# Kernel optimization log

Measured on AMD Instinct MI355X. Metric: run time of the kernel, lower is better.

## Reference

```python
import jax, jax.numpy as jnp
import numpy as np

HEAD_DIM = 32

def setup_inputs() -> dict:
    key = jax.random.key(0)
    ks = jax.random.split(key, 6)
    B, H, W, C = 16, 64, 64, 512
    ws = 8
    n_heads = C // HEAD_DIM
    return {
        "x": jax.random.normal(ks[0], (B, H, W, C), dtype=jnp.float32),
        "w_qkv": jax.random.normal(ks[1], (C, 3 * C), dtype=jnp.float32) * 0.02,
        "b_qkv": jnp.zeros((3 * C,), dtype=jnp.float32),
        "rel_pos": jax.random.normal(ks[2], ((2 * ws - 1) ** 2, n_heads), dtype=jnp.float32) * 0.02,
        "w_out": jax.random.normal(ks[3], (C, C), dtype=jnp.float32) * 0.02,
        "b_out": jnp.zeros((C,), dtype=jnp.float32),
        "window_size": ws,
    }

def _rel_pos_index(p):
    # static numpy computation, identical to torch buffer construction
    coords = np.stack(np.meshgrid(np.arange(p), np.arange(p), indexing='ij')).reshape(2, -1)
    rel = (coords[:, :, None] - coords[:, None, :]).transpose(1, 2, 0)
    rel[:, :, 0] += p - 1
    rel[:, :, 1] += p - 1
    rel[:, :, 0] *= 2 * p - 1
    return rel.sum(-1)  # (p*p, p*p)

def reference(x, w_qkv, b_qkv, rel_pos, w_out, b_out, window_size):
    B, H, W, C = x.shape
    p = int(window_size)
    n = p * p
    n_heads = rel_pos.shape[1]
    hd = C // n_heads
    shift = p // 2
    # type == 'W': cyclic shift before windowing
    xs = jnp.roll(x, shift=(-shift, -shift), axis=(1, 2))
    nh, nw = H // p, W // p
    # window partition -> (B*nh*nw, n, C)
    xw = xs.reshape(B, nh, p, nw, p, C).transpose(0, 1, 3, 2, 4, 5).reshape(B * nh * nw, n, C)
    qkv = xw @ w_qkv + b_qkv                      # (Bw, n, 3C)
    qkv = qkv.reshape(-1, n, 3, n_heads, hd).transpose(2, 0, 3, 1, 4)  # (3, Bw, h, n, hd)
    q, k, v = qkv[0], qkv[1], qkv[2]
    idx = _rel_pos_index(p)
    bias = rel_pos[idx.reshape(-1)].reshape(n, n, n_heads).transpose(2, 0, 1)  # (h, n, n)
    scale = hd ** -0.5
    attn = jnp.einsum('bhqd,bhkd->bhqk', q * scale, k) + bias[None]
    attn = jax.nn.softmax(attn, axis=-1)
    out = jnp.einsum('bhqk,bhkd->bhqd', attn, v)  # (Bw, h, n, hd)
    out = out.transpose(0, 2, 1, 3).reshape(-1, n, C)
    out = out @ w_out + b_out                     # (Bw, n, C_out)
    Co = out.shape[-1]
    out = out.reshape(B, nh, nw, p, p, Co).transpose(0, 1, 3, 2, 4, 5).reshape(B, H, W, Co)
    return jnp.roll(out, shift=(shift, shift), axis=(1, 2))
```

## Files before the change

kernel.cpp:

```cpp
#include <hip/hip_runtime.h>
#include <hip/hip_bf16.h>
#include <stdint.h>

typedef __hip_bfloat16 bf16;
typedef __attribute__((ext_vector_type(8))) short short8;
typedef __attribute__((ext_vector_type(4))) float f32x4;

#define NWIN 1024
#define NH 16
#define HD 32
#define SHIFT 4

#define GLOAD_LDS16(gptr, lptr)                                                      \
    __builtin_amdgcn_global_load_lds(                                                \
        (const __attribute__((address_space(1))) void*)(gptr),                       \
        (__attribute__((address_space(3))) void*)(lptr), 16, 0, 0)

__device__ __forceinline__ int row_to_pixel(int r) {
    int win = r >> 6, t = r & 63;
    int b = win >> 6, wy = (win >> 3) & 7, wx = win & 7;
    int h = ((wy << 3) + (t >> 3) + SHIFT) & 63;
    int w = ((wx << 3) + (t & 7) + SHIFT) & 63;
    return (((b << 6) | h) << 6) | w;
}

__device__ __forceinline__ short f2bf_bits(float f) {
    bf16 h = __float2bfloat16(f);
    return *reinterpret_cast<short*>(&h);
}

__global__ void transpose_f2b(const float* __restrict__ src, short* __restrict__ dst,
                              int K, int N) {
    int idx = blockIdx.x * 256 + threadIdx.x;
    if (idx >= K * N) return;
    int k = idx / N, n = idx - k * N;
    dst[n * K + k] = f2bf_bits(src[idx]);
}

__global__ __launch_bounds__(256)
void gather_cast(const float* __restrict__ x, short* __restrict__ a) {
    int chunk = blockIdx.x * 256 + threadIdx.x;
    int r = chunk >> 6, c8 = (chunk & 63) << 3;
    int pix = row_to_pixel(r);
    const float* src = x + pix * 512 + c8;
    float4 f0 = *(const float4*)src;
    float4 f1 = *(const float4*)(src + 4);
    short8 v;
    v[0] = f2bf_bits(f0.x); v[1] = f2bf_bits(f0.y);
    v[2] = f2bf_bits(f0.z); v[3] = f2bf_bits(f0.w);
    v[4] = f2bf_bits(f1.x); v[5] = f2bf_bits(f1.y);
    v[6] = f2bf_bits(f1.z); v[7] = f2bf_bits(f1.w);
    *(short8*)(a + r * 512 + c8) = v;
}

__global__ __launch_bounds__(256, 4)
void qkv_gemm(const bf16* __restrict__ a, const bf16* __restrict__ wT,
              const float* __restrict__ bqkv, bf16* __restrict__ qkv) {
    __shared__ __align__(16) short As[128 * 32];
    __shared__ __align__(16) short Bs[128 * 32];
    const int tid = threadIdx.x;
    const int lane = tid & 63, wave = tid >> 6;
    const int wr = wave >> 1, wc = wave & 1;
    const int h = blockIdx.x;
    const int v = (h & 7) * 768 + (h >> 3);
    const int by = v / 12, bx = v - by * 12;
    const int m0 = by * 128, n0 = bx * 128;

    const int lrow = lane >> 2, lc8 = (lane & 3) << 3;
    const short* agA0 = (const short*)a + (m0 + wave * 16 + lrow) * 512 + lc8;
    const short* agA1 = (const short*)a + (m0 + (wave + 4) * 16 + lrow) * 512 + lc8;
    const short* bgB0 = (const short*)wT + (n0 + wave * 16 + lrow) * 512 + lc8;
    const short* bgB1 = (const short*)wT + (n0 + (wave + 4) * 16 + lrow) * 512 + lc8;
    short* ldsA0 = As + wave * 512;
    short* ldsA1 = As + (wave + 4) * 512;
    short* ldsB0 = Bs + wave * 512;
    short* ldsB1 = Bs + (wave + 4) * 512;

    f32x4 acc[4][4] = {};
    for (int k0 = 0; k0 < 512; k0 += 32) {
        __syncthreads();
        GLOAD_LDS16(agA0 + k0, ldsA0);
        GLOAD_LDS16(agA1 + k0, ldsA1);
        GLOAD_LDS16(bgB0 + k0, ldsB0);
        GLOAD_LDS16(bgB1 + k0, ldsB1);
        __syncthreads();
        const int kk = (lane >> 4) << 3;
        short8 af[4], bfr[4];
#pragma unroll
        for (int mt = 0; mt < 4; ++mt)
            af[mt] = *(const short8*)&As[(wr * 64 + mt * 16 + (lane & 15)) * 32 + kk];
#pragma unroll
        for (int nt = 0; nt < 4; ++nt)
            bfr[nt] = *(const short8*)&Bs[(wc * 64 + nt * 16 + (lane & 15)) * 32 + kk];
#pragma unroll
        for (int mt = 0; mt < 4; ++mt)
#pragma unroll
            for (int nt = 0; nt < 4; ++nt)
                acc[mt][nt] = __builtin_amdgcn_mfma_f32_16x16x32_bf16(af[mt], bfr[nt],
                                                                      acc[mt][nt], 0, 0, 0);
    }

#pragma unroll
    for (int mt = 0; mt < 4; ++mt) {
        int r0 = m0 + wr * 64 + mt * 16 + ((lane >> 4) << 2);
        int win = r0 >> 6, t0 = r0 & 63;
#pragma unroll
        for (int nt = 0; nt < 4; ++nt) {
            int c = n0 + wc * 64 + nt * 16 + (lane & 15);
            int which = c >> 9, head = (c >> 5) & 15, d = c & 31;
            float bias = bqkv[c];
            float scale = (which == 0) ? 0.17677669529663689f : 1.0f;
            short* p = (short*)qkv + (((which * NWIN + win) * NH + head) * 64 + t0) * HD + d;
#pragma unroll
            for (int reg = 0; reg < 4; ++reg)
                p[reg * HD] = f2bf_bits((acc[mt][nt][reg] + bias) * scale);
        }
    }
}

__global__ __launch_bounds__(256, 4)
void attn_kernel(bf16* __restrict__ qkv, const float* __restrict__ relpos) {
    const int win = blockIdx.x, head = blockIdx.y;
    __shared__ __align__(16) short qs[64 * 40];
    __shared__ __align__(16) short ks[64 * 40];
    __shared__ __align__(16) short vT[32 * 72];
    __shared__ __align__(16) short Ps[64 * 72];
    __shared__ float rel[225];
    const int tid = threadIdx.x, lane = tid & 63, wave = tid >> 6;
    const int base = (win * NH + head) * 2048;
    const short* qg = (const short*)qkv + base;
    const short* kg = qg + NWIN * NH * 2048;
    const short* vg = kg + NWIN * NH * 2048;

    {
        int row = tid >> 2, c8 = (tid & 3) << 3;
        *(short8*)&qs[row * 40 + c8] = *(const short8*)(qg + row * 32 + c8);
        *(short8*)&ks[row * 40 + c8] = *(const short8*)(kg + row * 32 + c8);
        short8 vv = *(const short8*)(vg + row * 32 + c8);
#pragma unroll
        for (int e = 0; e < 8; ++e) vT[(c8 + e) * 72 + row] = vv[e];
    }
    if (tid < 225) rel[tid] = relpos[tid * 16 + head];
    __syncthreads();

    {
        const int kk = (lane >> 4) << 3;
        short8 aq = *(const short8*)&qs[(wave * 16 + (lane & 15)) * 40 + kk];
        f32x4 sacc[4];
#pragma unroll
        for (int nt = 0; nt < 4; ++nt) {
            short8 bk = *(const short8*)&ks[(nt * 16 + (lane & 15)) * 40 + kk];
            f32x4 z = {};
            sacc[nt] = __builtin_amdgcn_mfma_f32_16x16x32_bf16(aq, bk, z, 0, 0, 0);
        }
#pragma unroll
        for (int reg = 0; reg < 4; ++reg) {
            int qt = wave * 16 + ((lane >> 4) << 2) + reg;
            float pv[4];
            float m = -3e38f;
#pragma unroll
            for (int nt = 0; nt < 4; ++nt) {
                int kt = nt * 16 + (lane & 15);
                int idx = ((qt >> 3) - (kt >> 3) + 7) * 15 + ((qt & 7) - (kt & 7) + 7);
                pv[nt] = sacc[nt][reg] + rel[idx];
                m = fmaxf(m, pv[nt]);
            }
            m = fmaxf(m, __shfl_xor(m, 1));
            m = fmaxf(m, __shfl_xor(m, 2));
            m = fmaxf(m, __shfl_xor(m, 4));
            m = fmaxf(m, __shfl_xor(m, 8));
            float s = 0.f;
#pragma unroll
            for (int nt = 0; nt < 4; ++nt) { pv[nt] = __expf(pv[nt] - m); s += pv[nt]; }
            s += __shfl_xor(s, 1);
            s += __shfl_xor(s, 2);
            s += __shfl_xor(s, 4);
            s += __shfl_xor(s, 8);
            float inv = 1.f / s;
#pragma unroll
            for (int nt = 0; nt < 4; ++nt)
                Ps[qt * 72 + nt * 16 + (lane & 15)] = f2bf_bits(pv[nt] * inv);
        }
    }

    {
        f32x4 oacc[2] = {};
#pragma unroll
        for (int kstep = 0; kstep < 2; ++kstep) {
            const int kk = kstep * 32 + ((lane >> 4) << 3);
            short8 ap = *(const short8*)&Ps[(wave * 16 + (lane & 15)) * 72 + kk];
#pragma unroll
            for (int nt = 0; nt < 2; ++nt) {
                short8 bv = *(const short8*)&vT[(nt * 16 + (lane & 15)) * 72 + kk];
                oacc[nt] = __builtin_amdgcn_mfma_f32_16x16x32_bf16(ap, bv, oacc[nt], 0, 0, 0);
            }
        }
        short* og = (short*)qkv + base;
#pragma unroll
        for (int nt = 0; nt < 2; ++nt)
#pragma unroll
            for (int reg = 0; reg < 4; ++reg) {
                int t = wave * 16 + ((lane >> 4) << 2) + reg;
                int d = nt * 16 + (lane & 15);
                og[t * 32 + d] = f2bf_bits(oacc[nt][reg]);
            }
    }
}

__global__ __launch_bounds__(256, 4)
void out_gemm(const bf16* __restrict__ ain, const bf16* __restrict__ wT,
              const float* __restrict__ bout, float* __restrict__ out) {
    __shared__ __align__(16) short As[128 * 32];
    __shared__ __align__(16) short Bs[128 * 32];
    const int tid = threadIdx.x;
    const int lane = tid & 63, wave = tid >> 6;
    const int wr = wave >> 1, wc = wave & 1;
    const int h = blockIdx.x;
    const int v = (h & 7) * 256 + (h >> 3);
    const int bx = v & 3, by = v >> 2;
    const int m0 = by * 128, n0 = bx * 128;

    const int lrow = lane >> 2, lc8 = (lane & 3) << 3;
    const short* agA[2];
    const short* bgB[2];
    short* ldsA[2];
    short* ldsB[2];
#pragma unroll
    for (int s = 0; s < 2; ++s) {
        int c = wave + s * 4;
        int r = m0 + c * 16 + lrow, win = r >> 6, t = r & 63;
        agA[s] = (const short*)ain + win * 32768 + t * 32 + lc8;
        bgB[s] = (const short*)wT + (n0 + c * 16 + lrow) * 512 + lc8;
        ldsA[s] = As + c * 512;
        ldsB[s] = Bs + c * 512;
    }

    f32x4 acc[4][4] = {};
    for (int k0 = 0; k0 < 512; k0 += 32) {
        __syncthreads();
        GLOAD_LDS16(agA[0] + k0 * 64, ldsA[0]);
        GLOAD_LDS16(agA[1] + k0 * 64, ldsA[1]);
        GLOAD_LDS16(bgB[0] + k0, ldsB[0]);
        GLOAD_LDS16(bgB[1] + k0, ldsB[1]);
        __syncthreads();
        const int kk = (lane >> 4) << 3;
        short8 af[4], bfr[4];
#pragma unroll
        for (int mt = 0; mt < 4; ++mt)
            af[mt] = *(const short8*)&As[(wr * 64 + mt * 16 + (lane & 15)) * 32 + kk];
#pragma unroll
        for (int nt = 0; nt < 4; ++nt)
            bfr[nt] = *(const short8*)&Bs[(wc * 64 + nt * 16 + (lane & 15)) * 32 + kk];
#pragma unroll
        for (int mt = 0; mt < 4; ++mt)
#pragma unroll
            for (int nt = 0; nt < 4; ++nt)
                acc[mt][nt] = __builtin_amdgcn_mfma_f32_16x16x32_bf16(af[mt], bfr[nt],
                                                                      acc[mt][nt], 0, 0, 0);
    }

#pragma unroll
    for (int mt = 0; mt < 4; ++mt) {
        int r0 = m0 + wr * 64 + mt * 16 + ((lane >> 4) << 2);
        int pix0 = row_to_pixel(r0);
#pragma unroll
        for (int nt = 0; nt < 4; ++nt) {
            int c = n0 + wc * 64 + nt * 16 + (lane & 15);
            float bias = bout[c];
            float* po = out + pix0 * 512 + c;
#pragma unroll
            for (int reg = 0; reg < 4; ++reg)
                po[reg * 512] = acc[mt][nt][reg] + bias;
        }
    }
}

extern "C" void kernel_launch(void* const* d_in, const int* in_sizes, int n_in,
                              void* d_out, int out_size, void* d_ws, size_t ws_size,
                              hipStream_t stream) {
    const float* x       = (const float*)d_in[0];
    const float* w_qkv   = (const float*)d_in[1];
    const float* b_qkv   = (const float*)d_in[2];
    const float* rel_pos = (const float*)d_in[3];
    const float* w_out   = (const float*)d_in[4];
    const float* b_out   = (const float*)d_in[5];
    float* out = (float*)d_out;

    bf16* wqkvT  = (bf16*)d_ws;
    bf16* woutT  = wqkvT + 1536 * 512;
    bf16* qkvbuf = woutT + 512 * 512;

    short* agather = (short*)d_out;

    transpose_f2b<<<(512 * 1536 + 255) / 256, 256, 0, stream>>>(
        w_qkv, (short*)wqkvT, 512, 1536);
    transpose_f2b<<<(512 * 512 + 255) / 256, 256, 0, stream>>>(
        w_out, (short*)woutT, 512, 512);
    gather_cast<<<16384, 256, 0, stream>>>(x, agather);
    qkv_gemm<<<6144, 256, 0, stream>>>((const bf16*)agather, wqkvT, b_qkv, qkvbuf);
    attn_kernel<<<dim3(1024, 16), 256, 0, stream>>>(qkvbuf, rel_pos);
    out_gemm<<<2048, 256, 0, stream>>>(qkvbuf, woutT, b_out, out);
}
```

Before: 485.7 us.

## Enlarge QKV GEMM tiles to 256x256 with triple-buffered LDS pipeline and swizzle

The QKV projection GEMM moves from 128x128 tiles with 4 waves to 256x256 tiles with 8 waves, and LDS is triple-buffered so global-to-LDS loads run two k-steps ahead of the MFMA work. The LDS layout is XOR-swizzled to cut bank conflicts, and s_setprio raises priority around the MFMA block. Each block now does more reuse per byte loaded and pays for one barrier per k-step. The cost is one block per CU, more registers for the 8x4 accumulator tile, and less latency hiding from running multiple blocks at once.

```diff
diff --git a/kernel.cpp b/kernel.cpp
--- a/kernel.cpp
+++ b/kernel.cpp
@@ -53,67 +53,92 @@
     *(short8*)(a + r * 512 + c8) = v;
 }
 
-__global__ __launch_bounds__(256, 4)
+__global__ __launch_bounds__(512, 1)
 void qkv_gemm(const bf16* __restrict__ a, const bf16* __restrict__ wT,
               const float* __restrict__ bqkv, bf16* __restrict__ qkv) {
-    __shared__ __align__(16) short As[128 * 32];
-    __shared__ __align__(16) short Bs[128 * 32];
+    __shared__ __align__(16) short As[3 * 8192];
+    __shared__ __align__(16) short Bs[3 * 8192];
     const int tid = threadIdx.x;
     const int lane = tid & 63, wave = tid >> 6;
-    const int wr = wave >> 1, wc = wave & 1;
+    const int wm = wave >> 2, wn = wave & 3;
+    const int l15 = lane & 15;
     const int h = blockIdx.x;
-    const int v = (h & 7) * 768 + (h >> 3);
-    const int by = v / 12, bx = v - by * 12;
-    const int m0 = by * 128, n0 = bx * 128;
-
-    const int lrow = lane >> 2, lc8 = (lane & 3) << 3;
-    const short* agA0 = (const short*)a + (m0 + wave * 16 + lrow) * 512 + lc8;
-    const short* agA1 = (const short*)a + (m0 + (wave + 4) * 16 + lrow) * 512 + lc8;
-    const short* bgB0 = (const short*)wT + (n0 + wave * 16 + lrow) * 512 + lc8;
-    const short* bgB1 = (const short*)wT + (n0 + (wave + 4) * 16 + lrow) * 512 + lc8;
-    short* ldsA0 = As + wave * 512;
-    short* ldsA1 = As + (wave + 4) * 512;
-    short* ldsB0 = Bs + wave * 512;
-    short* ldsB1 = Bs + (wave + 4) * 512;
-
-    f32x4 acc[4][4] = {};
-    for (int k0 = 0; k0 < 512; k0 += 32) {
-        __syncthreads();
-        GLOAD_LDS16(agA0 + k0, ldsA0);
-        GLOAD_LDS16(agA1 + k0, ldsA1);
-        GLOAD_LDS16(bgB0 + k0, ldsB0);
-        GLOAD_LDS16(bgB1 + k0, ldsB1);
-        __syncthreads();
-        const int kk = (lane >> 4) << 3;
-        short8 af[4], bfr[4];
-#pragma unroll
-        for (int mt = 0; mt < 4; ++mt)
-            af[mt] = *(const short8*)&As[(wr * 64 + mt * 16 + (lane & 15)) * 32 + kk];
+    const int v = (h & 7) * 192 + (h >> 3);
+    const int by = v / 6, bx = v - by * 6;
+    const int m0 = by * 256, n0 = bx * 256;
+
+    const int lr = lane >> 2;
+    const int ss = (lane & 3) ^ (lr & 3);
+    const short* agA0 = (const short*)a + (size_t)(m0 + wave * 16 + lr) * 512 + ss * 8;
+    const short* bgB0 = (const short*)wT + (size_t)(n0 + wave * 16 + lr) * 512 + ss * 8;
+    const int koff = (((lane >> 4) ^ (lane & 3)) & 3) << 3;
+
+#define QKV_STAGE(tt, b) do {                                                        \
+        const short* _a0 = agA0 + (tt) * 32;                                         \
+        const short* _b0 = bgB0 + (tt) * 32;                                         \
+        GLOAD_LDS16(_a0,             &As[(b) * 8192 + wave * 512]);                  \
+        GLOAD_LDS16(_a0 + 128 * 512, &As[(b) * 8192 + (wave + 8) * 512]);            \
+        GLOAD_LDS16(_b0,             &Bs[(b) * 8192 + wave * 512]);                  \
+        GLOAD_LDS16(_b0 + 128 * 512, &Bs[(b) * 8192 + (wave + 8) * 512]);            \
+    } while (0)
+
+    QKV_STAGE(0, 0);
+    QKV_STAGE(1, 1);
+    asm volatile("s_waitcnt vmcnt(4)" ::: "memory");
+    __builtin_amdgcn_sched_barrier(0);
+    __builtin_amdgcn_s_barrier();
+    __builtin_amdgcn_sched_barrier(0);
+
+    f32x4 acc[8][4] = {};
+    int p = 0;
+#pragma unroll
+    for (int t = 0; t < 16; ++t) {
+        if (t < 14) {
+            int b2 = p + 2; if (b2 >= 3) b2 -= 3;
+            QKV_STAGE(t + 2, b2);
+        }
+        const short* Ab = &As[p * 8192];
+        const short* Bb = &Bs[p * 8192];
+        short8 af[8], bv[4];
+#pragma unroll
+        for (int mt = 0; mt < 8; ++mt)
+            af[mt] = *(const short8*)&Ab[(wm * 128 + mt * 16 + l15) * 32 + koff];
 #pragma unroll
         for (int nt = 0; nt < 4; ++nt)
-            bfr[nt] = *(const short8*)&Bs[(wc * 64 + nt * 16 + (lane & 15)) * 32 + kk];
-#pragma unroll
-        for (int mt = 0; mt < 4; ++mt)
+            bv[nt] = *(const short8*)&Bb[(wn * 64 + nt * 16 + l15) * 32 + koff];
+        __builtin_amdgcn_s_setprio(1);
+#pragma unroll
+        for (int mt = 0; mt < 8; ++mt)
 #pragma unroll
             for (int nt = 0; nt < 4; ++nt)
-                acc[mt][nt] = __builtin_amdgcn_mfma_f32_16x16x32_bf16(af[mt], bfr[nt],
+                acc[mt][nt] = __builtin_amdgcn_mfma_f32_16x16x32_bf16(af[mt], bv[nt],
                                                                       acc[mt][nt], 0, 0, 0);
-    }
-
-#pragma unroll
-    for (int mt = 0; mt < 4; ++mt) {
-        int r0 = m0 + wr * 64 + mt * 16 + ((lane >> 4) << 2);
+        __builtin_amdgcn_s_setprio(0);
+        if (t < 14)       asm volatile("s_waitcnt vmcnt(4)" ::: "memory");
+        else if (t == 14) asm volatile("s_waitcnt vmcnt(0)" ::: "memory");
+        if (t < 15) {
+            __builtin_amdgcn_sched_barrier(0);
+            __builtin_amdgcn_s_barrier();
+            __builtin_amdgcn_sched_barrier(0);
+        }
+        p = (p == 2) ? 0 : p + 1;
+    }
+#undef QKV_STAGE
+
+#pragma unroll
+    for (int mt = 0; mt < 8; ++mt) {
+        int r0 = m0 + wm * 128 + mt * 16 + ((lane >> 4) << 2);
         int win = r0 >> 6, t0 = r0 & 63;
 #pragma unroll
         for (int nt = 0; nt < 4; ++nt) {
-            int c = n0 + wc * 64 + nt * 16 + (lane & 15);
+            int c = n0 + wn * 64 + nt * 16 + l15;
             int which = c >> 9, head = (c >> 5) & 15, d = c & 31;
             float bias = bqkv[c];
             float scale = (which == 0) ? 0.17677669529663689f : 1.0f;
-            short* p = (short*)qkv + (((which * NWIN + win) * NH + head) * 64 + t0) * HD + d;
+            short* pq = (short*)qkv + (((which * NWIN + win) * NH + head) * 64 + t0) * HD + d;
 #pragma unroll
             for (int reg = 0; reg < 4; ++reg)
-                p[reg * HD] = f2bf_bits((acc[mt][nt][reg] + bias) * scale);
+                pq[reg * HD] = f2bf_bits((acc[mt][nt][reg] + bias) * scale);
         }
     }
 }
@@ -191,8 +216,8 @@
             short8 ap = *(const short8*)&Ps[(wave * 16 + (lane & 15)) * 72 + kk];
 #pragma unroll
             for (int nt = 0; nt < 2; ++nt) {
-                short8 bv = *(const short8*)&vT[(nt * 16 + (lane & 15)) * 72 + kk];
-                oacc[nt] = __builtin_amdgcn_mfma_f32_16x16x32_bf16(ap, bv, oacc[nt], 0, 0, 0);
+                short8 bvv = *(const short8*)&vT[(nt * 16 + (lane & 15)) * 72 + kk];
+                oacc[nt] = __builtin_amdgcn_mfma_f32_16x16x32_bf16(ap, bvv, oacc[nt], 0, 0, 0);
             }
         }
         short* og = (short*)qkv + base;
@@ -297,7 +322,7 @@
     transpose_f2b<<<(512 * 512 + 255) / 256, 256, 0, stream>>>(
         w_out, (short*)woutT, 512, 512);
     gather_cast<<<16384, 256, 0, stream>>>(x, agather);
-    qkv_gemm<<<6144, 256, 0, stream>>>((const bf16*)agather, wqkvT, b_qkv, qkvbuf);
+    qkv_gemm<<<1536, 512, 0, stream>>>((const bf16*)agather, wqkvT, b_qkv, qkvbuf);
     attn_kernel<<<dim3(1024, 16), 256, 0, stream>>>(qkvbuf, rel_pos);
     out_gemm<<<2048, 256, 0, stream>>>(qkvbuf, woutT, b_out, out);
 }
```

Measured after the change: 484.5 us. Within noise of the previous version (-0.3%).
